# Kernel tuning notes

Measured on AMD Instinct MI355X. Metric: run time of the kernel, lower is better.

## Reference

```python
import jax, jax.numpy as jnp
import numpy as np

D_MODEL = 256
NHEAD = 8
D_HEAD = D_MODEL // NHEAD
DIM_FF = 1024
B, L = 4, 16384
LN_EPS = 1e-5


def _layernorm(x, g, b):
    mu = jnp.mean(x, axis=-1, keepdims=True)
    var = jnp.mean((x - mu) ** 2, axis=-1, keepdims=True)
    return (x - mu) * jax.lax.rsqrt(var + LN_EPS) * g + b


def _phi(x):
    # elu(x) + 1
    return jnp.where(x > 0, x + 1.0, jnp.exp(x))


def setup_inputs() -> dict:
    key = jax.random.key(0)
    ks = jax.random.split(key, 16)
    s_in = 1.0 / np.sqrt(D_MODEL)
    s_ff = 1.0 / np.sqrt(DIM_FF)
    inp = {
        "x": jax.random.normal(ks[0], (B, L, D_MODEL), dtype=jnp.float32),
        "Wq": jax.random.normal(ks[1], (D_MODEL, D_MODEL), dtype=jnp.float32) * s_in,
        "bq": jnp.zeros((D_MODEL,), jnp.float32),
        "Wk": jax.random.normal(ks[2], (D_MODEL, D_MODEL), dtype=jnp.float32) * s_in,
        "bk": jnp.zeros((D_MODEL,), jnp.float32),
        "Wv": jax.random.normal(ks[3], (D_MODEL, D_MODEL), dtype=jnp.float32) * s_in,
        "bv": jnp.zeros((D_MODEL,), jnp.float32),
        "Wo": jax.random.normal(ks[4], (D_MODEL, D_MODEL), dtype=jnp.float32) * s_in,
        "bo": jnp.zeros((D_MODEL,), jnp.float32),
        "W1": jax.random.normal(ks[5], (D_MODEL, DIM_FF), dtype=jnp.float32) * s_in,
        "b1": jnp.zeros((DIM_FF,), jnp.float32),
        "W2": jax.random.normal(ks[6], (DIM_FF, D_MODEL), dtype=jnp.float32) * s_ff,
        "b2": jnp.zeros((D_MODEL,), jnp.float32),
        "ln1_g": jnp.ones((D_MODEL,), jnp.float32),
        "ln1_b": jnp.zeros((D_MODEL,), jnp.float32),
        "ln2_g": jnp.ones((D_MODEL,), jnp.float32),
        "ln2_b": jnp.zeros((D_MODEL,), jnp.float32),
    }
    return inp


def reference(x, Wq, bq, Wk, bk, Wv, bv, Wo, bo, W1, b1, W2, b2, ln1_g, ln1_b, ln2_g, ln2_b):
    Bq, Lq, _ = x.shape
    q = (x @ Wq + bq).reshape(Bq, Lq, NHEAD, D_HEAD)
    k = (x @ Wk + bk).reshape(Bq, Lq, NHEAD, D_HEAD)
    v = (x @ Wv + bv).reshape(Bq, Lq, NHEAD, D_HEAD)
    q_phi = _phi(q)
    k_phi = _phi(k)
    # kv: [B, H, d, e]
    kv = jnp.einsum("blhd,blhe->bhde", k_phi, v)
    k_sum = k_phi.sum(axis=1)  # [B, H, d]
    z = 1.0 / (jnp.einsum("blhd,bhd->blh", q_phi, k_sum) + 1e-6)
    out = jnp.einsum("blhd,bhde,blh->blhe", q_phi, kv, z)
    out = out.reshape(Bq, Lq, D_MODEL) @ Wo + bo
    x = _layernorm(x + out, ln1_g, ln1_b)
    ff = jax.nn.relu(x @ W1 + b1) @ W2 + b2
    x = _layernorm(x + ff, ln2_g, ln2_b)
    return x
```

## Files before the change

kernel.cpp:

```cpp
#include <hip/hip_runtime.h>
#include <hip/hip_bf16.h>
#include <math.h>

#define NTOK   65536
#define L_SEQ  16384

typedef __bf16 bf16_t;
typedef bf16_t bf16x8 __attribute__((ext_vector_type(8)));
typedef bf16_t bf16x4 __attribute__((ext_vector_type(4)));
typedef float  f32x4  __attribute__((ext_vector_type(4)));

__device__ inline float phi_f(float x) { return x > 0.f ? x + 1.f : __expf(x); }

__device__ inline float quad_sum(float v) {
    v += __shfl_xor(v, 1);
    v += __shfl_xor(v, 2);
    v += __shfl_xor(v, 4);
    v += __shfl_xor(v, 8);
    return v;
}

__device__ inline float ld_any(const void* p, size_t i, int f32) {
    return f32 ? ((const float*)p)[i] : (float)((const bf16_t*)p)[i];
}

__device__ inline void async_copy16(const bf16_t* g, bf16_t* l) {
    __builtin_amdgcn_global_load_lds(
        (const __attribute__((address_space(1))) unsigned int*)g,
        (__attribute__((address_space(3))) unsigned int*)l, 16, 0, 0);
}

__device__ inline void stage_swz(const bf16_t* __restrict__ g, bf16_t* lds,
                                 int tid, int nslot, int ulog2, int rowstride) {
    const int umask = (1 << ulog2) - 1;
    for (int s = tid; s < nslot; s += 256) {
        int n = s >> ulog2, j = s & umask;
        int u = j ^ (n & umask);
        async_copy16(g + (size_t)n * rowstride + u * 8, lds + (size_t)s * 8);
    }
}

__device__ inline bf16x8 rd_swz(const bf16_t* lds, int n, int u, int ulog2) {
    int j = u ^ (n & ((1 << ulog2) - 1));
    return *(const bf16x8*)&lds[(((size_t)n << ulog2) + j) * 8];
}

__device__ inline void ld_afrags(const bf16_t* __restrict__ tile, int row, int q8,
                                 bf16x8 a[8]) {
#pragma unroll
    for (int kk = 0; kk < 8; ++kk)
        a[kk] = *(const bf16x8*)&tile[(size_t)row * 256 + kk * 32 + q8];
}

__global__ __launch_bounds__(256) void k_detect(const void* __restrict__ xraw,
                                                int* __restrict__ flag) {
    __shared__ int bad;
    if (threadIdx.x == 0) bad = 0;
    __syncthreads();
    const bf16_t* xb = (const bf16_t*)xraw;
    int mybad = 0;
#pragma unroll
    for (int j = 0; j < 16; ++j) {
        float v = fabsf((float)xb[threadIdx.x + 256 * j]);
        if (!(v <= 1000.f)) mybad = 1;
    }
    if (mybad) atomicOr(&bad, 1);
    __syncthreads();
    if (threadIdx.x == 0) *flag = bad;
}

__global__ __launch_bounds__(256) void k_convert(const void* __restrict__ xraw,
                                                 const int* __restrict__ flag,
                                                 bf16_t* __restrict__ xbf) {
    const int f = *flag;
    size_t i = ((size_t)blockIdx.x * 256 + threadIdx.x) * 4;
    if (f) {
        f32x4 v = *(const f32x4*)((const float*)xraw + i);
        bf16x4 o;
#pragma unroll
        for (int j = 0; j < 4; ++j) o[j] = (bf16_t)v[j];
        *(bf16x4*)&xbf[i] = o;
    } else {
        *(bf16x4*)&xbf[i] = *(const bf16x4*)((const bf16_t*)xraw + i);
    }
}

__global__ __launch_bounds__(256) void k_prep(
    const void* __restrict__ Wq, const void* __restrict__ Wk,
    const void* __restrict__ Wv, const void* __restrict__ Wo,
    const void* __restrict__ W1, const void* __restrict__ W2,
    const void* __restrict__ bq, const void* __restrict__ bk,
    const void* __restrict__ bv, const void* __restrict__ bo,
    const void* __restrict__ b1, const void* __restrict__ b2,
    const void* __restrict__ g1, const void* __restrict__ be1,
    const void* __restrict__ g2, const void* __restrict__ be2,
    const int* __restrict__ flag,
    bf16_t* __restrict__ Wqkv_t, bf16_t* __restrict__ Wo_t,
    bf16_t* __restrict__ W1_t, bf16_t* __restrict__ W2_t,
    bf16_t* __restrict__ pbuf, float* __restrict__ kvbuf) {
    const int f = *flag;
    int idx = blockIdx.x * 256 + threadIdx.x;
    if (idx < 196608) {
        int n = idx >> 8, k = idx & 255;
        float v;
        if (n < 256)      v = ld_any(Wq, k * 256 + n, f);
        else if (n < 512) v = ld_any(Wk, k * 256 + (n - 256), f);
        else              v = ld_any(Wv, k * 256 + (n - 512), f);
        Wqkv_t[idx] = (bf16_t)v;
    } else if (idx < 262144) {
        int i = idx - 196608; int n = i >> 8, k = i & 255;
        Wo_t[i] = (bf16_t)ld_any(Wo, k * 256 + n, f);
    } else if (idx < 524288) {
        int i = idx - 262144; int n = i >> 8, k = i & 255;
        W1_t[i] = (bf16_t)ld_any(W1, k * 1024 + n, f);
    } else if (idx < 786432) {
        int i = idx - 524288; int n = i >> 10, k = i & 1023;
        W2_t[i] = (bf16_t)ld_any(W2, k * 256 + n, f);
    } else if (idx < 820224) {
        kvbuf[idx - 786432] = 0.f;
    } else if (idx < 823552) {
        int i = idx - 820224;
        float v;
        if (i < 256)        v = ld_any(bq, i, f);
        else if (i < 512)   v = ld_any(bk, i - 256, f);
        else if (i < 768)   v = ld_any(bv, i - 512, f);
        else if (i < 1024)  v = ld_any(bo, i - 768, f);
        else if (i < 2048)  v = ld_any(b1, i - 1024, f);
        else if (i < 2304)  v = ld_any(b2, i - 2048, f);
        else if (i < 2560)  v = ld_any(g1, i - 2304, f);
        else if (i < 2816)  v = ld_any(be1, i - 2560, f);
        else if (i < 3072)  v = ld_any(g2, i - 2816, f);
        else                v = ld_any(be2, i - 3072, f);
        pbuf[i] = (bf16_t)v;
    }
}

__global__ __launch_bounds__(256, 4) void k_qkv(
    const bf16_t* __restrict__ x, const bf16_t* __restrict__ Wqkv_t,
    const bf16_t* __restrict__ pbuf,
    bf16_t* __restrict__ q_phi, bf16_t* __restrict__ k_phi,
    bf16_t* __restrict__ v_out) {
    const int mt = blockIdx.x, nt = blockIdx.y;
    const int tid = threadIdx.x, wave = tid >> 6, lane = tid & 63;
    const int l15 = lane & 15, quad = lane >> 4, q8 = quad * 8;
    __shared__ __align__(16) bf16_t bs[128 * 256];
    const int m0 = mt * 64;
    bf16x8 a[8];
    ld_afrags(x + (size_t)m0 * 256, wave * 16 + l15, q8, a);
    stage_swz(Wqkv_t + (size_t)nt * 128 * 256, bs, tid, 4096, 5, 256);
    __syncthreads();
    f32x4 acc[8] = {};
#pragma unroll
    for (int kk = 0; kk < 8; ++kk) {
#pragma unroll
        for (int s = 0; s < 8; ++s) {
            bf16x8 b = rd_swz(bs, s * 16 + l15, kk * 4 + quad, 5);
            acc[s] = __builtin_amdgcn_mfma_f32_16x16x32_bf16(a[kk], b, acc[s], 0, 0, 0);
        }
    }
#pragma unroll
    for (int s = 0; s < 8; ++s) {
        int ng = nt * 128 + s * 16 + l15;
        bf16_t* dst = ng < 256 ? q_phi : (ng < 512 ? k_phi : v_out);
        int nl = ng & 255;
        float bias = (float)pbuf[(ng < 256 ? 0 : (ng < 512 ? 256 : 512)) + nl];
#pragma unroll
        for (int r = 0; r < 4; ++r) {
            int m = m0 + wave * 16 + quad * 4 + r;
            float val = acc[s][r] + bias;
            if (ng < 512) val = phi_f(val);
            dst[(size_t)m * 256 + nl] = (bf16_t)val;
        }
    }
}

__global__ __launch_bounds__(256) void k_kvsum(
    const bf16_t* __restrict__ k_phi, const bf16_t* __restrict__ v_in,
    float* __restrict__ kvbuf) {
    const int bid = blockIdx.x;
    const int bh = bid >> 6, ck = bid & 63;
    const int b = bh >> 3, h = bh & 7;
    const int tid = threadIdx.x;
    __shared__ float ks[32][33], vs[32][33];
    const size_t base = ((size_t)b * L_SEQ + ck * 256) * 256 + h * 32;
    const int row = tid >> 3, c4 = (tid & 7) * 4;
    const int d = row, e4 = c4;
    float acc[4] = {}, ksacc = 0.f;
    for (int it = 0; it < 8; ++it) {
        bf16x4 kk4 = *(const bf16x4*)&k_phi[base + (size_t)(it * 32 + row) * 256 + c4];
        bf16x4 vv4 = *(const bf16x4*)&v_in[base + (size_t)(it * 32 + row) * 256 + c4];
#pragma unroll
        for (int j = 0; j < 4; ++j) { ks[row][c4 + j] = (float)kk4[j]; vs[row][c4 + j] = (float)vv4[j]; }
        __syncthreads();
#pragma unroll
        for (int ii = 0; ii < 32; ++ii) {
            float kd = ks[ii][d];
            ksacc += kd;
#pragma unroll
            for (int j = 0; j < 4; ++j) acc[j] += kd * vs[ii][e4 + j];
        }
        __syncthreads();
    }
    float* kvdst = kvbuf + (size_t)bh * 1056;
#pragma unroll
    for (int j = 0; j < 4; ++j) atomicAdd(&kvdst[(e4 + j) * 32 + d], acc[j]);
    if ((tid & 7) == 0) atomicAdd(&kvdst[1024 + d], ksacc);
}

__global__ __launch_bounds__(256) void k_kvprep(const float* __restrict__ kvbuf,
                                                bf16_t* __restrict__ kvbf) {
    int idx = blockIdx.x * 256 + threadIdx.x;
    int bh = idx >> 8, r4 = (idx & 255) * 4;
    f32x4 v = *(const f32x4*)&kvbuf[(size_t)bh * 1056 + r4];
    bf16x4 o;
#pragma unroll
    for (int j = 0; j < 4; ++j) o[j] = (bf16_t)v[j];
    *(bf16x4*)&kvbf[(size_t)bh * 1024 + r4] = o;
}

__global__ __launch_bounds__(256, 3) void k_attn_wo_ln1(
    const bf16_t* __restrict__ q_phi, const bf16_t* __restrict__ kvbf,
    const float* __restrict__ kvbuf, const bf16_t* __restrict__ Wo_t,
    const bf16_t* __restrict__ pbuf, const void* __restrict__ xraw,
    const int* __restrict__ flag, bf16_t* __restrict__ x1) {
    const int f = *flag;
    const int mt = blockIdx.x;
    const int tid = threadIdx.x, wave = tid >> 6, lane = tid & 63;
    const int l15 = lane & 15, quad = lane >> 4, q8 = quad * 8;
    __shared__ __align__(16) bf16_t sm0[8192];
    __shared__ __align__(16) bf16_t sm1[16896];
    const int m0 = mt * 64;
    const int b = m0 >> 14;
    bf16x8 a[8];
    ld_afrags(q_phi + (size_t)m0 * 256, wave * 16 + l15, q8, a);
    stage_swz(Wo_t, sm0, tid, 1024, 5, 256);
    bf16_t* hs = sm1 + wave * (16 * 264);
    const bf16_t* kvb = kvbf + (size_t)b * 8192;
    const float*  ksb = kvbuf + (size_t)b * 8448;
#pragma unroll
    for (int h = 0; h < 8; ++h) {
        f32x4 ks0 = *(const f32x4*)&ksb[h * 1056 + 1024 + q8];
        f32x4 ks1 = *(const f32x4*)&ksb[h * 1056 + 1024 + q8 + 4];
        float den = 0.f;
#pragma unroll
        for (int j = 0; j < 4; ++j) den += (float)a[h][j] * ks0[j];
#pragma unroll
        for (int j = 0; j < 4; ++j) den += (float)a[h][4 + j] * ks1[j];
        den += __shfl_xor(den, 16);
        den += __shfl_xor(den, 32);
        float z = 1.f / (den + 1e-6f);
        float zr[4];
#pragma unroll
        for (int r = 0; r < 4; ++r) zr[r] = __shfl(z, quad * 4 + r, 16);
        bf16x8 b0 = *(const bf16x8*)&kvb[h * 1024 + l15 * 32 + q8];
        bf16x8 b1 = *(const bf16x8*)&kvb[h * 1024 + (16 + l15) * 32 + q8];
        f32x4 at0 = {}, at1 = {};
        at0 = __builtin_amdgcn_mfma_f32_16x16x32_bf16(a[h], b0, at0, 0, 0, 0);
        at1 = __builtin_amdgcn_mfma_f32_16x16x32_bf16(a[h], b1, at1, 0, 0, 0);
#pragma unroll
        for (int r = 0; r < 4; ++r) {
            hs[(quad * 4 + r) * 264 + h * 32 + l15]      = (bf16_t)(at0[r] * zr[r]);
            hs[(quad * 4 + r) * 264 + h * 32 + 16 + l15] = (bf16_t)(at1[r] * zr[r]);
        }
    }
    bf16x8 a2[8];
#pragma unroll
    for (int kk = 0; kk < 8; ++kk)
        a2[kk] = *(const bf16x8*)&hs[l15 * 264 + kk * 32 + q8];
    __syncthreads();
    f32x4 acc[16] = {};
    for (int nc = 0; nc < 8; ++nc) {
        if (nc < 7) stage_swz(Wo_t + (size_t)(nc + 1) * 32 * 256,
                              (nc & 1) ? sm0 : sm1, tid, 1024, 5, 256);
        const bf16_t* buf = (nc & 1) ? sm1 : sm0;
#pragma unroll
        for (int kk = 0; kk < 8; ++kk) {
#pragma unroll
            for (int s = 0; s < 2; ++s) {
                bf16x8 bb = rd_swz(buf, s * 16 + l15, kk * 4 + quad, 5);
                acc[nc * 2 + s] = __builtin_amdgcn_mfma_f32_16x16x32_bf16(a2[kk], bb, acc[nc * 2 + s], 0, 0, 0);
            }
        }
        __syncthreads();
    }
    float s1[4] = {}, s2[4] = {};
#pragma unroll
    for (int s = 0; s < 16; ++s) {
        int n = s * 16 + l15;
        float bias = (float)pbuf[768 + n];
#pragma unroll
        for (int r = 0; r < 4; ++r) {
            int m = m0 + wave * 16 + quad * 4 + r;
            float val = acc[s][r] + bias + ld_any(xraw, (size_t)m * 256 + n, f);
            acc[s][r] = val;
            s1[r] += val; s2[r] += val * val;
        }
    }
#pragma unroll
    for (int r = 0; r < 4; ++r) {
        float ts = quad_sum(s1[r]), ts2 = quad_sum(s2[r]);
        float mu = ts * (1.f / 256.f);
        float rs = rsqrtf(ts2 * (1.f / 256.f) - mu * mu + 1e-5f);
        s1[r] = mu; s2[r] = rs;
    }
#pragma unroll
    for (int s = 0; s < 16; ++s) {
        int n = s * 16 + l15;
        float gn = (float)pbuf[2304 + n], bn = (float)pbuf[2560 + n];
#pragma unroll
        for (int r = 0; r < 4; ++r) {
            int m = m0 + wave * 16 + quad * 4 + r;
            x1[(size_t)m * 256 + n] = (bf16_t)((acc[s][r] - s1[r]) * s2[r] * gn + bn);
        }
    }
}

__global__ __launch_bounds__(256, 3) void k_ff_ln2(
    const bf16_t* __restrict__ x1, const bf16_t* __restrict__ W1_t,
    const bf16_t* __restrict__ W2_t, const bf16_t* __restrict__ pbuf,
    const int* __restrict__ flag, void* __restrict__ out) {
    const int f32o = *flag;
    const int mt = blockIdx.x;
    const int tid = threadIdx.x, wave = tid >> 6, lane = tid & 63;
    const int l15 = lane & 15, quad = lane >> 4, q8 = quad * 8;
    __shared__ __align__(16) bf16_t w1s[8192];
    __shared__ __align__(16) bf16_t w2s[8192];
    __shared__ __align__(16) bf16_t hs[4][16][40];
    const int m0 = mt * 64;
    bf16x8 a[8];
    ld_afrags(x1 + (size_t)m0 * 256, wave * 16 + l15, q8, a);
    stage_swz(W1_t, w1s, tid, 1024, 5, 256);
    __syncthreads();
    f32x4 acc[16] = {};
    for (int ch = 0; ch < 32; ++ch) {
        stage_swz(W2_t + ch * 32, w2s, tid, 1024, 2, 1024);
        f32x4 hacc[2] = {};
#pragma unroll
        for (int kk = 0; kk < 8; ++kk) {
#pragma unroll
            for (int s = 0; s < 2; ++s) {
                bf16x8 b = rd_swz(w1s, s * 16 + l15, kk * 4 + quad, 5);
                hacc[s] = __builtin_amdgcn_mfma_f32_16x16x32_bf16(a[kk], b, hacc[s], 0, 0, 0);
            }
        }
#pragma unroll
        for (int s = 0; s < 2; ++s) {
            float bias = (float)pbuf[1024 + ch * 32 + s * 16 + l15];
#pragma unroll
            for (int r = 0; r < 4; ++r) {
                float val = hacc[s][r] + bias;
                hs[wave][quad * 4 + r][s * 16 + l15] = (bf16_t)(val > 0.f ? val : 0.f);
            }
        }
        bf16x8 a2 = *(const bf16x8*)&hs[wave][l15][q8];
        __syncthreads();
        if (ch < 31) stage_swz(W1_t + (size_t)(ch + 1) * 32 * 256, w1s, tid, 1024, 5, 256);
#pragma unroll
        for (int s = 0; s < 16; ++s) {
            bf16x8 b0 = rd_swz(w2s, s * 16 + l15, quad, 2);
            acc[s] = __builtin_amdgcn_mfma_f32_16x16x32_bf16(a2, b0, acc[s], 0, 0, 0);
        }
        __syncthreads();
    }
    float s1[4] = {}, s2[4] = {};
#pragma unroll
    for (int s = 0; s < 16; ++s) {
        int n = s * 16 + l15;
        float bias = (float)pbuf[2048 + n];
#pragma unroll
        for (int r = 0; r < 4; ++r) {
            int m = m0 + wave * 16 + quad * 4 + r;
            float val = acc[s][r] + bias + (float)x1[(size_t)m * 256 + n];
            acc[s][r] = val;
            s1[r] += val; s2[r] += val * val;
        }
    }
#pragma unroll
    for (int r = 0; r < 4; ++r) {
        float ts = quad_sum(s1[r]), ts2 = quad_sum(s2[r]);
        float mu = ts * (1.f / 256.f);
        float rs = rsqrtf(ts2 * (1.f / 256.f) - mu * mu + 1e-5f);
        s1[r] = mu; s2[r] = rs;
    }
#pragma unroll
    for (int s = 0; s < 16; ++s) {
        int n = s * 16 + l15;
        float gn = (float)pbuf[2816 + n], bn = (float)pbuf[3072 + n];
#pragma unroll
        for (int r = 0; r < 4; ++r) {
            int m = m0 + wave * 16 + quad * 4 + r;
            float val = (acc[s][r] - s1[r]) * s2[r] * gn + bn;
            if (f32o) ((float*)out)[(size_t)m * 256 + n] = val;
            else      ((bf16_t*)out)[(size_t)m * 256 + n] = (bf16_t)val;
        }
    }
}

extern "C" void kernel_launch(void* const* d_in, const int* in_sizes, int n_in,
                              void* d_out, int out_size, void* d_ws, size_t ws_size,
                              hipStream_t stream) {
    char* ws = (char*)d_ws;
    int*    flag   = (int*)ws;
    bf16_t* xbf    = (bf16_t*)(ws + 256);
    bf16_t* Wqkv_t = (bf16_t*)(ws + 33554688);
    bf16_t* Wo_t   = (bf16_t*)(ws + 33947904);
    bf16_t* W1_t   = (bf16_t*)(ws + 34078976);
    bf16_t* W2_t   = (bf16_t*)(ws + 34603264);
    bf16_t* pbuf   = (bf16_t*)(ws + 35127552);
    float*  kvbuf  = (float*)(ws + 35134208);
    bf16_t* bufQ   = (bf16_t*)(ws + 35269376);
    bf16_t* bufK   = bufQ + (size_t)NTOK * 256;
    bf16_t* bufV   = bufK + (size_t)NTOK * 256;
    bf16_t* kvbf   = bufV;
    bf16_t* bufX1  = bufQ;

    k_detect<<<1, 256, 0, stream>>>(d_in[0], flag);
    k_convert<<<16384, 256, 0, stream>>>(d_in[0], flag, xbf);
    k_prep<<<3217, 256, 0, stream>>>(d_in[1], d_in[3], d_in[5], d_in[7],
                                     d_in[9], d_in[11],
                                     d_in[2], d_in[4], d_in[6], d_in[8],
                                     d_in[10], d_in[12],
                                     d_in[13], d_in[14], d_in[15], d_in[16],
                                     flag, Wqkv_t, Wo_t, W1_t, W2_t, pbuf, kvbuf);
    k_qkv<<<dim3(1024, 6), 256, 0, stream>>>(xbf, Wqkv_t, pbuf, bufQ, bufK, bufV);
    k_kvsum<<<2048, 256, 0, stream>>>(bufK, bufV, kvbuf);
    k_kvprep<<<32, 256, 0, stream>>>(kvbuf, kvbf);
    k_attn_wo_ln1<<<1024, 256, 0, stream>>>(bufQ, kvbf, kvbuf, Wo_t, pbuf,
                                            d_in[0], flag, bufX1);
    k_ff_ln2<<<1024, 256, 0, stream>>>(bufX1, W1_t, W2_t, pbuf, flag, d_out);
}
```

Measured before the change: 427.9 us.

## Double-buffer W1/W2 chunks in FF kernel and use conflict-free W2 swizzle

The FF+LN2 kernel now keeps two LDS buffers for W1 and W2 chunks. It prefetches chunk ch+1 asynchronously while computing chunk ch, and drops one of the two barriers per iteration. The W2 staging uses a new swizzle that spreads rows over 8 slots to cut LDS bank conflicts on the B-fragment reads. Shared memory per block doubles to about 69KB, which may lower occupancy below the 3 blocks per CU the launch bounds request.

```diff
diff --git a/kernel.cpp b/kernel.cpp
--- a/kernel.cpp
+++ b/kernel.cpp
@@ -43,6 +43,24 @@
 __device__ inline bf16x8 rd_swz(const bf16_t* lds, int n, int u, int ulog2) {
     int j = u ^ (n & ((1 << ulog2) - 1));
     return *(const bf16x8*)&lds[(((size_t)n << ulog2) + j) * 8];
+}
+
+__device__ inline void stage_w2ff(const bf16_t* __restrict__ W2_t, int ch,
+                                  bf16_t* lds, int tid) {
+    for (int S = tid; S < 1024; S += 256) {
+        int r = S >> 3, phys = S & 7;
+        int u = phys ^ (r & 7);
+        int n = ((u >> 2) << 7) + r;
+        int ks = u & 3;
+        async_copy16(W2_t + (size_t)n * 1024 + ch * 32 + ks * 8, lds + (size_t)S * 8);
+    }
+}
+
+__device__ inline bf16x8 rd_w2ff(const bf16_t* lds, int n, int quad) {
+    int r = n & 127;
+    int u = ((n >> 7) << 2) + quad;
+    int phys = u ^ (r & 7);
+    return *(const bf16x8*)&lds[(size_t)(r * 8 + phys) * 8];
 }
 
 __device__ inline void ld_afrags(const bf16_t* __restrict__ tile, int row, int q8,
@@ -323,23 +341,28 @@
     const int mt = blockIdx.x;
     const int tid = threadIdx.x, wave = tid >> 6, lane = tid & 63;
     const int l15 = lane & 15, quad = lane >> 4, q8 = quad * 8;
-    __shared__ __align__(16) bf16_t w1s[8192];
-    __shared__ __align__(16) bf16_t w2s[8192];
+    __shared__ __align__(16) bf16_t w1s[2][8192];
+    __shared__ __align__(16) bf16_t w2s[2][8192];
     __shared__ __align__(16) bf16_t hs[4][16][40];
     const int m0 = mt * 64;
     bf16x8 a[8];
     ld_afrags(x1 + (size_t)m0 * 256, wave * 16 + l15, q8, a);
-    stage_swz(W1_t, w1s, tid, 1024, 5, 256);
+    stage_swz(W1_t, w1s[0], tid, 1024, 5, 256);
+    stage_w2ff(W2_t, 0, w2s[0], tid);
     __syncthreads();
     f32x4 acc[16] = {};
     for (int ch = 0; ch < 32; ++ch) {
-        stage_swz(W2_t + ch * 32, w2s, tid, 1024, 2, 1024);
+        const int cur = ch & 1;
+        if (ch < 31) {
+            stage_swz(W1_t + (size_t)(ch + 1) * 32 * 256, w1s[cur ^ 1], tid, 1024, 5, 256);
+            stage_w2ff(W2_t, ch + 1, w2s[cur ^ 1], tid);
+        }
         f32x4 hacc[2] = {};
 #pragma unroll
         for (int kk = 0; kk < 8; ++kk) {
 #pragma unroll
             for (int s = 0; s < 2; ++s) {
-                bf16x8 b = rd_swz(w1s, s * 16 + l15, kk * 4 + quad, 5);
+                bf16x8 b = rd_swz(w1s[cur], s * 16 + l15, kk * 4 + quad, 5);
                 hacc[s] = __builtin_amdgcn_mfma_f32_16x16x32_bf16(a[kk], b, hacc[s], 0, 0, 0);
             }
         }
@@ -353,11 +376,9 @@
             }
         }
         bf16x8 a2 = *(const bf16x8*)&hs[wave][l15][q8];
-        __syncthreads();
-        if (ch < 31) stage_swz(W1_t + (size_t)(ch + 1) * 32 * 256, w1s, tid, 1024, 5, 256);
 #pragma unroll
         for (int s = 0; s < 16; ++s) {
-            bf16x8 b0 = rd_swz(w2s, s * 16 + l15, quad, 2);
+            bf16x8 b0 = rd_w2ff(w2s[cur], s * 16 + l15, quad);
             acc[s] = __builtin_amdgcn_mfma_f32_16x16x32_bf16(a2, b0, acc[s], 0, 0, 0);
         }
         __syncthreads();
```

Measured after the change: 432.3 us. About the same (+1.0%).
